# Kernel optimization log

Hardware: AMD Instinct MI355X
Metric: run time of the kernel (lower is better)

## Reference

```python
import jax, jax.numpy as jnp
import numpy as np

B, S, D_IN, D_OUT, H = 2, 2048, 1024, 1024, 16
HD = D_OUT // H  # head dim = 64


def setup_inputs() -> dict:
    key = jax.random.key(0)
    ks = jax.random.split(key, 9)
    s_in = 1.0 / np.sqrt(D_IN)
    s_out = 1.0 / np.sqrt(D_OUT)
    return {
        "X": jax.random.normal(ks[0], (B, S, D_IN), dtype=jnp.float32),
        "Wq": jax.random.uniform(ks[1], (D_OUT, D_IN), jnp.float32, -s_in, s_in),
        "bq": jax.random.uniform(ks[2], (D_OUT,), jnp.float32, -s_in, s_in),
        "Wk": jax.random.uniform(ks[3], (D_OUT, D_IN), jnp.float32, -s_in, s_in),
        "bk": jax.random.uniform(ks[4], (D_OUT,), jnp.float32, -s_in, s_in),
        "Wv": jax.random.uniform(ks[5], (D_OUT, D_IN), jnp.float32, -s_in, s_in),
        "bv": jax.random.uniform(ks[6], (D_OUT,), jnp.float32, -s_in, s_in),
        "Wo": jax.random.uniform(ks[7], (D_OUT, D_OUT), jnp.float32, -s_out, s_out),
        "bo": jax.random.uniform(ks[8], (D_OUT,), jnp.float32, -s_out, s_out),
    }


def reference(X, Wq, bq, Wk, bk, Wv, bv, Wo, bo):
    scale = jnp.asarray(HD ** 0.5, X.dtype)  # self.dim = sqrt(head_dim)
    q = X @ Wq.T + bq  # [B,S,D_OUT]
    k = X @ Wk.T + bk
    v = X @ Wv.T + bv
    # split heads: b s (h d) -> b h s d
    q = q.reshape(B, S, H, HD).transpose(0, 2, 1, 3)
    k = k.reshape(B, S, H, HD).transpose(0, 2, 1, 3)
    v = v.reshape(B, S, H, HD).transpose(0, 2, 1, 3)
    scores = jnp.einsum('bhsd,bhtd->bhst', q, k) / scale  # [B,H,S,S]
    causal = jnp.triu(jnp.ones((S, S), dtype=bool), k=1)
    scores = jnp.where(causal, -jnp.inf, scores)
    weights = jax.nn.softmax(scores, axis=-1)
    out = jnp.einsum('bhst,bhtd->bhsd', weights, v)  # [B,H,S,HD]
    out = out.transpose(0, 2, 1, 3).reshape(B, S, D_OUT)  # b h s d -> b s (h d)
    return out @ Wo.T + bo
```

## Files before the change

### kernel.cpp

```cpp
#include <hip/hip_runtime.h>
#include <hip/hip_bf16.h>

typedef __bf16 bf16_t;
typedef __bf16 bf16x8 __attribute__((ext_vector_type(8)));
typedef float  f32x4  __attribute__((ext_vector_type(4)));
typedef unsigned short ushort_t;

#define MFMA16(a, b, c) __builtin_amdgcn_mfma_f32_16x16x32_bf16((a), (b), (c), 0, 0, 0)
#define GLDS16(g, l) __builtin_amdgcn_global_load_lds( \
    (const __attribute__((address_space(1))) unsigned int*)(g), \
    (__attribute__((address_space(3))) unsigned int*)(l), 16, 0, 0)

#define WAITCNT_VM(n)  (0x0F70 | (n))
#define WAITCNT_LGKM0  0xC07F

#define MEMFENCE asm volatile("" ::: "memory")

#define QSCALE 0.18033688f

__global__ __launch_bounds__(256) void cvt_all(
    const void* __restrict__ X,  const void* __restrict__ W0, const void* __restrict__ W1,
    const void* __restrict__ W2, const void* __restrict__ W3,
    const void* __restrict__ c0, const void* __restrict__ c1,
    const void* __restrict__ c2, const void* __restrict__ c3,
    bf16_t* __restrict__ Xb, bf16_t* __restrict__ Wb, float* __restrict__ biasF,
    int* __restrict__ flag)
{
    const int tid  = threadIdx.x;
    const int lane = tid & 63;
    const ushort_t u = ((const ushort_t*)X)[2 * lane];
    const int e = (u >> 7) & 0xFF;
    const int f = (__ballot(e >= 0xA0) != 0ull) ? 1 : 0;

    const int bid = blockIdx.x;
    if (bid >= 4096) {
        if (bid == 4096 && tid == 0) *flag = f;
        const int idx = ((bid - 4096) * 256 + tid) * 8;
        const int w = idx >> 10, off = idx & 1023;
        const void* src = (w == 0) ? c0 : (w == 1) ? c1 : (w == 2) ? c2 : c3;
        #pragma unroll
        for (int r = 0; r < 8; ++r)
            biasF[idx + r] = f ? ((const float*)src)[off + r]
                               : (float)((const bf16_t*)src)[off + r];
        return;
    }

    const long long i = (long long)bid * 2048 + tid * 8;
    const void* src;
    bf16_t* dst;
    long long off;
    if (i < 4194304) { src = X; dst = Xb; off = i; }
    else {
        const int w = (int)((i - 4194304) >> 20);
        off = (i - 4194304) & 1048575;
        src = (w == 0) ? W0 : (w == 1) ? W1 : (w == 2) ? W2 : W3;
        dst = Wb + (size_t)w * 1048576;
    }
    if (f) {
        const float* s = (const float*)src + off;
        const float4 a = *(const float4*)(s);
        const float4 b = *(const float4*)(s + 4);
        bf16x8 o;
        o[0] = (bf16_t)a.x; o[1] = (bf16_t)a.y; o[2] = (bf16_t)a.z; o[3] = (bf16_t)a.w;
        o[4] = (bf16_t)b.x; o[5] = (bf16_t)b.y; o[6] = (bf16_t)b.z; o[7] = (bf16_t)b.w;
        *(bf16x8*)(dst + off) = o;
    } else {
        *(bf16x8*)(dst + off) = *(const bf16x8*)((const bf16_t*)src + off);
    }
}

__global__ __launch_bounds__(512, 2) void gemm256(
    const bf16_t* __restrict__ A,
    const bf16_t* __restrict__ W0, const bf16_t* __restrict__ W1, const bf16_t* __restrict__ W2,
    const float* __restrict__ b0, const float* __restrict__ b1, const float* __restrict__ b2,
    bf16_t* __restrict__ C, bf16_t* __restrict__ Vt)
{
    __shared__ bf16_t Ash[4][256 * 32];
    __shared__ bf16_t Bsh[4][256 * 32];

    const int tid  = threadIdx.x;
    const int wid  = tid >> 6;
    const int lane = tid & 63;
    const int g    = lane >> 4;
    const int c    = lane & 15;

    const int m0  = blockIdx.x * 256;
    const int n0  = blockIdx.y * 256;
    const int mat = n0 >> 10;
    const bf16_t* W  = (mat == 0) ? W0 : (mat == 1) ? W1 : W2;
    const float*  bs = (mat == 0) ? b0 : (mat == 1) ? b1 : b2;
    const int nw = n0 & 1023;

    const int srow = lane >> 2;
    const int sblk = (lane & 3) ^ ((lane >> 3) & 3);
    const bf16_t* Ag = A + (size_t)(m0 + wid * 32 + srow) * 1024 + sblk * 8;
    const bf16_t* Wg = W + (size_t)(nw + wid * 32 + srow) * 1024 + sblk * 8;

    const int waveM = (wid >> 2) * 128;
    const int waveN = (wid & 3) * 64;
    const int fblk  = (g ^ ((c >> 1) & 3)) * 8;

    f32x4 acc[8][4] = {};

    auto stageA = [&](int H, int q) {
        GLDS16(Ag + (size_t)(q * 16) * 1024 + H * 32, &Ash[H & 3][(wid * 32 + q * 16) * 32]);
    };
    auto stageB = [&](int H, int q) {
        GLDS16(Wg + (size_t)(q * 16) * 1024 + H * 32, &Bsh[H & 3][(wid * 32 + q * 16) * 32]);
    };

    for (int H = 0; H < 3; ++H) {
        stageA(H, 0); stageA(H, 1); stageB(H, 0); stageB(H, 1);
    }
    __builtin_amdgcn_s_waitcnt(WAITCNT_VM(8));
    __builtin_amdgcn_s_barrier();
    MEMFENCE;

    #pragma unroll 4
    for (int H = 0; H < 32; ++H) {
        const int buf = H & 3;
        const bf16_t* As = Ash[buf];
        const bf16_t* Bs = Bsh[buf];

        bf16x8 bfr[4], af[8];
        #pragma unroll
        for (int j = 0; j < 4; ++j)
            bfr[j] = *(const bf16x8*)(&Bs[(waveN + j * 16 + c) * 32 + fblk]);
        #pragma unroll
        for (int i = 0; i < 8; ++i)
            af[i] = *(const bf16x8*)(&As[(waveM + i * 16 + c) * 32 + fblk]);

        if (H < 29) { stageA(H + 3, 0); stageA(H + 3, 1); stageB(H + 3, 0); stageB(H + 3, 1); }

        __builtin_amdgcn_s_setprio(1);
        #pragma unroll
        for (int i = 0; i < 8; ++i)
            #pragma unroll
            for (int j = 0; j < 4; ++j)
                acc[i][j] = MFMA16(af[i], bfr[j], acc[i][j]);
        __builtin_amdgcn_s_setprio(0);

        MEMFENCE;
        __builtin_amdgcn_s_waitcnt(WAITCNT_LGKM0);
        if (H < 29)       __builtin_amdgcn_s_waitcnt(WAITCNT_VM(8));
        else if (H == 29) __builtin_amdgcn_s_waitcnt(WAITCNT_VM(4));
        else if (H == 30) __builtin_amdgcn_s_waitcnt(WAITCNT_VM(0));
        __builtin_amdgcn_s_barrier();
        MEMFENCE;
    }

    if (mat == 2) {
        #pragma unroll
        for (int j = 0; j < 4; ++j) {
            const int col  = n0 + waveN + j * 16 + c;
            const int hcol = col & 1023;
            const float bv = bs[hcol];
            const int h = hcol >> 6, d = hcol & 63;
            #pragma unroll
            for (int i = 0; i < 8; ++i) {
                const int row = m0 + waveM + i * 16 + g * 4;
                const int bb = row >> 11, s = row & 2047;
                bf16_t pk[4];
                #pragma unroll
                for (int r = 0; r < 4; ++r) pk[r] = (bf16_t)(acc[i][j][r] + bv);
                *(uint2*)(&Vt[(((size_t)bb * 16 + h) * 64 + d) * 2048 + s]) = *(uint2*)pk;
            }
        }
        return;
    }

    const float os = (mat == 0) ? QSCALE : 1.0f;
    #pragma unroll
    for (int j = 0; j < 4; ++j) {
        const int col = n0 + waveN + j * 16 + c;
        const float bv = bs[col & 1023];
        #pragma unroll
        for (int i = 0; i < 8; ++i) {
            const int row = m0 + waveM + i * 16 + g * 4;
            #pragma unroll
            for (int r = 0; r < 4; ++r)
                C[(size_t)(row + r) * 3072 + col] = (bf16_t)((acc[i][j][r] + bv) * os);
        }
    }
}

template<int TM>
__global__ __launch_bounds__(256, 2) void gemm_nt(
    const bf16_t* __restrict__ A,
    const bf16_t* __restrict__ W0, const bf16_t* __restrict__ W1, const bf16_t* __restrict__ W2,
    const float* __restrict__ b0, const float* __restrict__ b1, const float* __restrict__ b2,
    void* __restrict__ C, int ldc, bf16_t* __restrict__ Vt, int fuse_vt,
    const int* __restrict__ flag, int is_out)
{
    constexpr int MI = TM / 32;
    constexpr int G  = (TM == 128) ? 4 : 3;
    __shared__ bf16_t Ash[3][TM * 32];
    __shared__ bf16_t Bsh[3][128 * 32];

    const int f32out = is_out ? *flag : 0;

    const int tid  = threadIdx.x;
    const int wid  = tid >> 6;
    const int lane = tid & 63;
    const int g    = lane >> 4;
    const int c    = lane & 15;

    const int m0  = blockIdx.x * TM;
    const int n0  = blockIdx.y * 128;
    const int mat = n0 >> 10;
    const bf16_t* W  = (mat == 0) ? W0 : (mat == 1) ? W1 : W2;
    const float*  bs = (mat == 0) ? b0 : (mat == 1) ? b1 : b2;
    const int nw = n0 & 1023;

    const int srow = lane >> 2;
    const int sblk = (lane & 3) ^ ((lane >> 3) & 3);
    const bf16_t* Ag = A + (size_t)(m0 + wid * (TM / 4) + srow) * 1024 + sblk * 8;
    const bf16_t* Wg = W + (size_t)(nw + wid * 32 + srow) * 1024 + sblk * 8;

    const int waveM = (wid >> 1) * (TM / 2);
    const int waveN = (wid & 1) * 64;

    f32x4 acc[MI][4] = {};
    const int fblk = (g ^ ((c >> 1) & 3)) * 8;

    auto stage = [&](int t, int buf) {
        const int k0 = t * 32;
        bf16_t* As = &Ash[buf][(wid * (TM / 4)) * 32];
        bf16_t* Bs = &Bsh[buf][(wid * 32) * 32];
        GLDS16(Ag + k0, As);
        if (TM == 128) GLDS16(Ag + (size_t)16 * 1024 + k0, As + 16 * 32);
        GLDS16(Wg + k0, Bs);
        GLDS16(Wg + (size_t)16 * 1024 + k0, Bs + 16 * 32);
    };

    stage(0, 0);
    stage(1, 1);
    __builtin_amdgcn_s_waitcnt(WAITCNT_VM(G));
    __builtin_amdgcn_s_barrier();
    MEMFENCE;

    #pragma unroll 3
    for (int k = 0; k < 32; ++k) {
        const int cur = k % 3;
        bf16x8 af[MI], bfr[4];
        #pragma unroll
        for (int i = 0; i < MI; ++i)
            af[i] = *(const bf16x8*)(&Ash[cur][(waveM + i * 16 + c) * 32 + fblk]);
        #pragma unroll
        for (int j = 0; j < 4; ++j)
            bfr[j] = *(const bf16x8*)(&Bsh[cur][(waveN + j * 16 + c) * 32 + fblk]);

        if (k < 30) stage(k + 2, (k + 2) % 3);

        #pragma unroll
        for (int i = 0; i < MI; ++i)
            #pragma unroll
            for (int j = 0; j < 4; ++j)
                acc[i][j] = MFMA16(af[i], bfr[j], acc[i][j]);

        MEMFENCE;
        __builtin_amdgcn_s_waitcnt(WAITCNT_LGKM0);
        if (k < 30)       __builtin_amdgcn_s_waitcnt(WAITCNT_VM(G));
        else if (k == 30) __builtin_amdgcn_s_waitcnt(WAITCNT_VM(0));
        __builtin_amdgcn_s_barrier();
        MEMFENCE;
    }

    if (fuse_vt && mat == 2) {
        #pragma unroll
        for (int j = 0; j < 4; ++j) {
            const int col  = n0 + waveN + j * 16 + c;
            const int hcol = col & 1023;
            const float bv = bs[hcol];
            const int h = hcol >> 6, d = hcol & 63;
            #pragma unroll
            for (int i = 0; i < MI; ++i) {
                const int row = m0 + waveM + i * 16 + g * 4;
                const int bb = row >> 11, s = row & 2047;
                bf16_t pk[4];
                #pragma unroll
                for (int r = 0; r < 4; ++r) pk[r] = (bf16_t)(acc[i][j][r] + bv);
                *(uint2*)(&Vt[(((size_t)bb * 16 + h) * 64 + d) * 2048 + s]) = *(uint2*)pk;
            }
        }
        return;
    }

    const float oscale = (fuse_vt && mat == 0) ? QSCALE : 1.0f;
    #pragma unroll
    for (int j = 0; j < 4; ++j) {
        const int col = n0 + waveN + j * 16 + c;
        const float bv = bs[col & 1023];
        #pragma unroll
        for (int i = 0; i < MI; ++i) {
            const int row = m0 + waveM + i * 16 + g * 4;
            #pragma unroll
            for (int r = 0; r < 4; ++r) {
                const float val = (acc[i][j][r] + bv) * oscale;
                const size_t idx = (size_t)(row + r) * ldc + col;
                if (f32out) ((float*)C)[idx] = val;
                else        ((bf16_t*)C)[idx] = (bf16_t)val;
            }
        }
    }
}

__global__ __launch_bounds__(256, 4) void attn_kernel(
    const bf16_t* __restrict__ QKV, const bf16_t* __restrict__ Vt,
    bf16_t* __restrict__ O)
{
    __shared__ bf16_t Ksh[64][72];
    __shared__ bf16_t Vsh[64][72];
    __shared__ bf16_t Psh[4][16][72];

    const int tid  = threadIdx.x;
    const int wid  = tid >> 6;
    const int lane = tid & 63;
    const int g    = lane >> 4;
    const int c    = lane & 15;

    const int bh = blockIdx.y;
    const int b  = bh >> 4, h = bh & 15;
    const int qt = (bh < 16) ? blockIdx.x : (31 - blockIdx.x);
    const int q0 = qt * 64;
    const int nt = qt + 1;

    bf16x8 aq[2];
    {
        const bf16_t* qp = QKV + (size_t)(b * 2048 + q0 + wid * 16 + c) * 3072 + h * 64;
        aq[0] = *(const bf16x8*)(qp + g * 8);
        aq[1] = *(const bf16x8*)(qp + 32 + g * 8);
    }

    float li[4] = {};
    f32x4 o[4]  = {};

    const int sr  = tid >> 2;
    const int sc0 = (tid & 3) * 16;
    const bf16_t* Kg = QKV + (size_t)(b * 2048 + sr) * 3072 + 1024 + h * 64 + sc0;
    const bf16_t* Vg = Vt + ((size_t)bh * 64 + sr) * 2048 + sc0;

    uint4 kr0 = *(const uint4*)(Kg);
    uint4 kr1 = *(const uint4*)(Kg + 8);
    uint4 vr0 = *(const uint4*)(Vg);
    uint4 vr1 = *(const uint4*)(Vg + 8);

    for (int jt = 0; jt < nt; ++jt) {
        *(uint4*)(&Ksh[sr][sc0])     = kr0;
        *(uint4*)(&Ksh[sr][sc0 + 8]) = kr1;
        *(uint4*)(&Vsh[sr][sc0])     = vr0;
        *(uint4*)(&Vsh[sr][sc0 + 8]) = vr1;
        __syncthreads();

        if (jt + 1 < nt) {
            const size_t ko = (size_t)(jt + 1) * 64 * 3072;
            kr0 = *(const uint4*)(Kg + ko);
            kr1 = *(const uint4*)(Kg + ko + 8);
            vr0 = *(const uint4*)(Vg + (jt + 1) * 64);
            vr1 = *(const uint4*)(Vg + (jt + 1) * 64 + 8);
        }

        f32x4 s[4] = {};
        #pragma unroll
        for (int n = 0; n < 4; ++n)
            #pragma unroll
            for (int kb = 0; kb < 2; ++kb) {
                const bf16x8 kf = *(const bf16x8*)(&Ksh[n * 16 + c][kb * 32 + g * 8]);
                s[n] = MFMA16(aq[kb], kf, s[n]);
            }

        if (jt == nt - 1) {
            const int j0 = jt * 64;
            const int qrow = q0 + wid * 16 + g * 4;
            #pragma unroll
            for (int n = 0; n < 4; ++n)
                #pragma unroll
                for (int r = 0; r < 4; ++r)
                    if (j0 + n * 16 + c > qrow + r) s[n][r] = -1e30f;
        }

        #pragma unroll
        for (int n = 0; n < 4; ++n)
            #pragma unroll
            for (int r = 0; r < 4; ++r) {
                const float p = __builtin_amdgcn_exp2f(s[n][r]);
                li[r] += p;
                Psh[wid][g * 4 + r][n * 16 + c] = (bf16_t)p;
            }
        __builtin_amdgcn_wave_barrier();

        #pragma unroll
        for (int kb = 0; kb < 2; ++kb) {
            const bf16x8 ap = *(const bf16x8*)(&Psh[wid][c][kb * 32 + g * 8]);
            #pragma unroll
            for (int d = 0; d < 4; ++d) {
                const bf16x8 vf = *(const bf16x8*)(&Vsh[d * 16 + c][kb * 32 + g * 8]);
                o[d] = MFMA16(ap, vf, o[d]);
            }
        }
        __syncthreads();
    }

    #pragma unroll
    for (int off = 1; off < 16; off <<= 1)
        #pragma unroll
        for (int r = 0; r < 4; ++r)
            li[r] += __shfl_xor(li[r], off, 64);

    const int orow = b * 2048 + q0 + wid * 16 + g * 4;
    #pragma unroll
    for (int r = 0; r < 4; ++r) {
        const float inv = 1.0f / li[r];
        #pragma unroll
        for (int d = 0; d < 4; ++d)
            O[(size_t)(orow + r) * 1024 + h * 64 + d * 16 + c] = (bf16_t)(o[d][r] * inv);
    }
}

extern "C" void kernel_launch(void* const* d_in, const int* in_sizes, int n_in,
                              void* d_out, int out_size, void* d_ws, size_t ws_size,
                              hipStream_t stream)
{
    const void* X  = d_in[0];
    const void* Wq = d_in[1];  const void* bq = d_in[2];
    const void* Wk = d_in[3];  const void* bk = d_in[4];
    const void* Wv = d_in[5];  const void* bv = d_in[6];
    const void* Wo = d_in[7];  const void* bo = d_in[8];

    int*    flag  = (int*)d_ws;
    float*  biasF = (float*)((char*)d_ws + 16);
    bf16_t* Xb    = (bf16_t*)((char*)d_ws + 16 + 16384);
    bf16_t* Wb    = Xb  + (size_t)4096 * 1024;
    bf16_t* QKV   = Wb  + (size_t)4 * 1024 * 1024;
    bf16_t* Vt    = QKV + (size_t)4096 * 3072;
    bf16_t* Ao    = Vt  + (size_t)4096 * 1024;

    const size_t MW = (size_t)1024 * 1024;

    cvt_all<<<4098, 256, 0, stream>>>(X, Wq, Wk, Wv, Wo, bq, bk, bv, bo,
                                      Xb, Wb, biasF, flag);

    gemm256<<<dim3(16, 12), 512, 0, stream>>>(
        Xb, Wb, Wb + MW, Wb + 2 * MW,
        biasF, biasF + 1024, biasF + 2048, QKV, Vt);
    attn_kernel<<<dim3(32, 32), 256, 0, stream>>>(QKV, Vt, Ao);
    gemm_nt<64><<<dim3(64, 8), 256, 0, stream>>>(
        Ao, Wb + 3 * MW, Wb + 3 * MW, Wb + 3 * MW,
        biasF + 3072, biasF + 3072, biasF + 3072, d_out, 1024, (bf16_t*)nullptr, 0, flag, 1);
}
```

Baseline: 197.8 us.

## Restructure GEMM and attention pipelines to two-stage steps with double-buffered K/V

Both GEMM kernels now process two K-steps per barrier using four LDS buffers, prefetching two steps ahead and waiting for all loads once per pair. This halves the barrier count at the cost of a shallower per-step prefetch distance. The second GEMM's occupancy hint rises from 2 to 3 blocks per CU and gains MFMA priority boosts. The attention kernel double-buffers its K/V shared tiles so the next tile is written after compute, removing one __syncthreads per iteration, and raises priority around its MFMAs.

```diff
diff --git a/kernel.cpp b/kernel.cpp
--- a/kernel.cpp
+++ b/kernel.cpp
@@ -109,42 +109,60 @@
         GLDS16(Wg + (size_t)(q * 16) * 1024 + H * 32, &Bsh[H & 3][(wid * 32 + q * 16) * 32]);
     };
 
-    for (int H = 0; H < 3; ++H) {
-        stageA(H, 0); stageA(H, 1); stageB(H, 0); stageB(H, 1);
-    }
-    __builtin_amdgcn_s_waitcnt(WAITCNT_VM(8));
+    stageA(0, 0); stageA(0, 1); stageB(0, 0); stageB(0, 1);
+    stageA(1, 0); stageA(1, 1); stageB(1, 0); stageB(1, 1);
+    __builtin_amdgcn_s_waitcnt(WAITCNT_VM(0));
     __builtin_amdgcn_s_barrier();
     MEMFENCE;
 
-    #pragma unroll 4
-    for (int H = 0; H < 32; ++H) {
-        const int buf = H & 3;
-        const bf16_t* As = Ash[buf];
-        const bf16_t* Bs = Bsh[buf];
-
-        bf16x8 bfr[4], af[8];
-        #pragma unroll
-        for (int j = 0; j < 4; ++j)
-            bfr[j] = *(const bf16x8*)(&Bs[(waveN + j * 16 + c) * 32 + fblk]);
-        #pragma unroll
-        for (int i = 0; i < 8; ++i)
-            af[i] = *(const bf16x8*)(&As[(waveM + i * 16 + c) * 32 + fblk]);
-
-        if (H < 29) { stageA(H + 3, 0); stageA(H + 3, 1); stageB(H + 3, 0); stageB(H + 3, 1); }
-
-        __builtin_amdgcn_s_setprio(1);
-        #pragma unroll
-        for (int i = 0; i < 8; ++i)
+    #pragma unroll 2
+    for (int s = 0; s < 16; ++s) {
+        const int h0 = 2 * s, h1 = 2 * s + 1;
+        if (s < 15) {
+            stageA(h0 + 2, 0); stageA(h0 + 2, 1); stageB(h0 + 2, 0); stageB(h0 + 2, 1);
+            stageA(h1 + 2, 0); stageA(h1 + 2, 1); stageB(h1 + 2, 0); stageB(h1 + 2, 1);
+        }
+
+        {
+            const bf16_t* As = Ash[h0 & 3];
+            const bf16_t* Bs = Bsh[h0 & 3];
+            bf16x8 bfr[4], af[8];
             #pragma unroll
             for (int j = 0; j < 4; ++j)
-                acc[i][j] = MFMA16(af[i], bfr[j], acc[i][j]);
-        __builtin_amdgcn_s_setprio(0);
+                bfr[j] = *(const bf16x8*)(&Bs[(waveN + j * 16 + c) * 32 + fblk]);
+            #pragma unroll
+            for (int i = 0; i < 8; ++i)
+                af[i] = *(const bf16x8*)(&As[(waveM + i * 16 + c) * 32 + fblk]);
+            __builtin_amdgcn_s_setprio(1);
+            #pragma unroll
+            for (int i = 0; i < 8; ++i)
+                #pragma unroll
+                for (int j = 0; j < 4; ++j)
+                    acc[i][j] = MFMA16(af[i], bfr[j], acc[i][j]);
+            __builtin_amdgcn_s_setprio(0);
+        }
+        {
+            const bf16_t* As = Ash[h1 & 3];
+            const bf16_t* Bs = Bsh[h1 & 3];
+            bf16x8 bfr[4], af[8];
+            #pragma unroll
+            for (int j = 0; j < 4; ++j)
+                bfr[j] = *(const bf16x8*)(&Bs[(waveN + j * 16 + c) * 32 + fblk]);
+            #pragma unroll
+            for (int i = 0; i < 8; ++i)
+                af[i] = *(const bf16x8*)(&As[(waveM + i * 16 + c) * 32 + fblk]);
+            __builtin_amdgcn_s_setprio(1);
+            #pragma unroll
+            for (int i = 0; i < 8; ++i)
+                #pragma unroll
+                for (int j = 0; j < 4; ++j)
+                    acc[i][j] = MFMA16(af[i], bfr[j], acc[i][j]);
+            __builtin_amdgcn_s_setprio(0);
+        }
 
         MEMFENCE;
         __builtin_amdgcn_s_waitcnt(WAITCNT_LGKM0);
-        if (H < 29)       __builtin_amdgcn_s_waitcnt(WAITCNT_VM(8));
-        else if (H == 29) __builtin_amdgcn_s_waitcnt(WAITCNT_VM(4));
-        else if (H == 30) __builtin_amdgcn_s_waitcnt(WAITCNT_VM(0));
+        if (s < 15) __builtin_amdgcn_s_waitcnt(WAITCNT_VM(0));
         __builtin_amdgcn_s_barrier();
         MEMFENCE;
     }
@@ -185,7 +203,7 @@
 }
 
 template<int TM>
-__global__ __launch_bounds__(256, 2) void gemm_nt(
+__global__ __launch_bounds__(256, 3) void gemm_nt(
     const bf16_t* __restrict__ A,
     const bf16_t* __restrict__ W0, const bf16_t* __restrict__ W1, const bf16_t* __restrict__ W2,
     const float* __restrict__ b0, const float* __restrict__ b1, const float* __restrict__ b2,
@@ -193,9 +211,8 @@
     const int* __restrict__ flag, int is_out)
 {
     constexpr int MI = TM / 32;
-    constexpr int G  = (TM == 128) ? 4 : 3;
-    __shared__ bf16_t Ash[3][TM * 32];
-    __shared__ bf16_t Bsh[3][128 * 32];
+    __shared__ bf16_t Ash[4][TM * 32];
+    __shared__ bf16_t Bsh[4][128 * 32];
 
     const int f32out = is_out ? *flag : 0;
 
@@ -223,8 +240,9 @@
     f32x4 acc[MI][4] = {};
     const int fblk = (g ^ ((c >> 1) & 3)) * 8;
 
-    auto stage = [&](int t, int buf) {
+    auto stage = [&](int t) {
         const int k0 = t * 32;
+        const int buf = t & 3;
         bf16_t* As = &Ash[buf][(wid * (TM / 4)) * 32];
         bf16_t* Bs = &Bsh[buf][(wid * 32) * 32];
         GLDS16(Ag + k0, As);
@@ -233,35 +251,39 @@
         GLDS16(Wg + (size_t)16 * 1024 + k0, Bs + 16 * 32);
     };
 
-    stage(0, 0);
-    stage(1, 1);
-    __builtin_amdgcn_s_waitcnt(WAITCNT_VM(G));
+    stage(0);
+    stage(1);
+    __builtin_amdgcn_s_waitcnt(WAITCNT_VM(0));
     __builtin_amdgcn_s_barrier();
     MEMFENCE;
 
-    #pragma unroll 3
-    for (int k = 0; k < 32; ++k) {
-        const int cur = k % 3;
-        bf16x8 af[MI], bfr[4];
-        #pragma unroll
-        for (int i = 0; i < MI; ++i)
-            af[i] = *(const bf16x8*)(&Ash[cur][(waveM + i * 16 + c) * 32 + fblk]);
-        #pragma unroll
-        for (int j = 0; j < 4; ++j)
-            bfr[j] = *(const bf16x8*)(&Bsh[cur][(waveN + j * 16 + c) * 32 + fblk]);
-
-        if (k < 30) stage(k + 2, (k + 2) % 3);
-
-        #pragma unroll
-        for (int i = 0; i < MI; ++i)
+    #pragma unroll 2
+    for (int s = 0; s < 16; ++s) {
+        const int t0 = 2 * s, t1 = 2 * s + 1;
+        if (s < 15) { stage(t0 + 2); stage(t1 + 2); }
+
+        #pragma unroll
+        for (int half = 0; half < 2; ++half) {
+            const int cur = (2 * s + half) & 3;
+            bf16x8 af[MI], bfr[4];
+            #pragma unroll
+            for (int i = 0; i < MI; ++i)
+                af[i] = *(const bf16x8*)(&Ash[cur][(waveM + i * 16 + c) * 32 + fblk]);
             #pragma unroll
             for (int j = 0; j < 4; ++j)
-                acc[i][j] = MFMA16(af[i], bfr[j], acc[i][j]);
+                bfr[j] = *(const bf16x8*)(&Bsh[cur][(waveN + j * 16 + c) * 32 + fblk]);
+            __builtin_amdgcn_s_setprio(1);
+            #pragma unroll
+            for (int i = 0; i < MI; ++i)
+                #pragma unroll
+                for (int j = 0; j < 4; ++j)
+                    acc[i][j] = MFMA16(af[i], bfr[j], acc[i][j]);
+            __builtin_amdgcn_s_setprio(0);
+        }
 
         MEMFENCE;
         __builtin_amdgcn_s_waitcnt(WAITCNT_LGKM0);
-        if (k < 30)       __builtin_amdgcn_s_waitcnt(WAITCNT_VM(G));
-        else if (k == 30) __builtin_amdgcn_s_waitcnt(WAITCNT_VM(0));
+        if (s < 15) __builtin_amdgcn_s_waitcnt(WAITCNT_VM(0));
         __builtin_amdgcn_s_barrier();
         MEMFENCE;
     }
@@ -309,8 +331,8 @@
     const bf16_t* __restrict__ QKV, const bf16_t* __restrict__ Vt,
     bf16_t* __restrict__ O)
 {
-    __shared__ bf16_t Ksh[64][72];
-    __shared__ bf16_t Vsh[64][72];
+    __shared__ bf16_t Ksh[2][64][72];
+    __shared__ bf16_t Vsh[2][64][72];
     __shared__ bf16_t Psh[4][16][72];
 
     const int tid  = threadIdx.x;
@@ -345,12 +367,14 @@
     uint4 vr0 = *(const uint4*)(Vg);
     uint4 vr1 = *(const uint4*)(Vg + 8);
 
+    *(uint4*)(&Ksh[0][sr][sc0])     = kr0;
+    *(uint4*)(&Ksh[0][sr][sc0 + 8]) = kr1;
+    *(uint4*)(&Vsh[0][sr][sc0])     = vr0;
+    *(uint4*)(&Vsh[0][sr][sc0 + 8]) = vr1;
+    __syncthreads();
+
     for (int jt = 0; jt < nt; ++jt) {
-        *(uint4*)(&Ksh[sr][sc0])     = kr0;
-        *(uint4*)(&Ksh[sr][sc0 + 8]) = kr1;
-        *(uint4*)(&Vsh[sr][sc0])     = vr0;
-        *(uint4*)(&Vsh[sr][sc0 + 8]) = vr1;
-        __syncthreads();
+        const int cur = jt & 1;
 
         if (jt + 1 < nt) {
             const size_t ko = (size_t)(jt + 1) * 64 * 3072;
@@ -361,13 +385,15 @@
         }
 
         f32x4 s[4] = {};
+        __builtin_amdgcn_s_setprio(1);
         #pragma unroll
         for (int n = 0; n < 4; ++n)
             #pragma unroll
             for (int kb = 0; kb < 2; ++kb) {
-                const bf16x8 kf = *(const bf16x8*)(&Ksh[n * 16 + c][kb * 32 + g * 8]);
+                const bf16x8 kf = *(const bf16x8*)(&Ksh[cur][n * 16 + c][kb * 32 + g * 8]);
                 s[n] = MFMA16(aq[kb], kf, s[n]);
             }
+        __builtin_amdgcn_s_setprio(0);
 
         if (jt == nt - 1) {
             const int j0 = jt * 64;
@@ -389,14 +415,23 @@
             }
         __builtin_amdgcn_wave_barrier();
 
+        __builtin_amdgcn_s_setprio(1);
         #pragma unroll
         for (int kb = 0; kb < 2; ++kb) {
             const bf16x8 ap = *(const bf16x8*)(&Psh[wid][c][kb * 32 + g * 8]);
             #pragma unroll
             for (int d = 0; d < 4; ++d) {
-                const bf16x8 vf = *(const bf16x8*)(&Vsh[d * 16 + c][kb * 32 + g * 8]);
+                const bf16x8 vf = *(const bf16x8*)(&Vsh[cur][d * 16 + c][kb * 32 + g * 8]);
                 o[d] = MFMA16(ap, vf, o[d]);
             }
+        }
+        __builtin_amdgcn_s_setprio(0);
+
+        if (jt + 1 < nt) {
+            *(uint4*)(&Ksh[cur ^ 1][sr][sc0])     = kr0;
+            *(uint4*)(&Ksh[cur ^ 1][sr][sc0 + 8]) = kr1;
+            *(uint4*)(&Vsh[cur ^ 1][sr][sc0])     = vr0;
+            *(uint4*)(&Vsh[cur ^ 1][sr][sc0 + 8]) = vr1;
         }
         __syncthreads();
     }
```

Result: slower. 222.2 us (+12.3%).
